# Optimization experiments

Hardware: AMD Instinct MI355X
Metric: run time of the kernel (lower is better)

## Reference

```python
import jax, jax.numpy as jnp
import numpy as np

B, H, KVH, HD, S = 16, 32, 8, 128, 4096
D = H * HD  # 4096
Q = 1  # decode: one query token per batch element


def rotate_half(x):
    half = x.shape[-1] // 2
    return jnp.concatenate([-x[..., half:], x[..., :half]], axis=-1)


def setup_inputs() -> dict:
    key = jax.random.key(0)
    ks = jax.random.split(key, 8)
    hidden_states = jax.random.normal(ks[0], (B, Q, D), dtype=jnp.float32)
    current_steps = jax.random.randint(ks[1], (B,), 0, S - 1)
    # additive causal mask per batch: positions <= current_step visible
    pos = jnp.arange(S)[None, :]
    attention_mask = jnp.where(pos <= current_steps[:, None], 0.0, -1e9).astype(jnp.float32)[:, None, None, :]  # [B,1,1,S]
    # RoPE cos/sin at each batch element's current position
    inv_freq = 1.0 / (10000.0 ** (jnp.arange(0, HD, 2, dtype=jnp.float32) / HD))
    ang = current_steps[:, None].astype(jnp.float32) * inv_freq[None, :]  # [B, HD/2]
    ang = jnp.concatenate([ang, ang], axis=-1)  # [B, HD]
    cos = jnp.cos(ang)[:, None, None, :]  # [B,1,1,HD]
    sin = jnp.sin(ang)[:, None, None, :]
    past_key = jax.random.normal(ks[2], (B, KVH, S, HD), dtype=jnp.float32)
    past_value = jax.random.normal(ks[3], (B, KVH, S, HD), dtype=jnp.float32)
    sc = 1.0 / np.sqrt(D)
    Wq = jax.random.normal(ks[4], (D, H * HD), dtype=jnp.float32) * sc
    Wk = jax.random.normal(ks[5], (D, KVH * HD), dtype=jnp.float32) * sc
    Wv = jax.random.normal(ks[6], (D, KVH * HD), dtype=jnp.float32) * sc
    Wo = jax.random.normal(ks[7], (H * HD, D), dtype=jnp.float32) * sc
    return dict(hidden_states=hidden_states, attention_mask=attention_mask,
                current_steps=current_steps, cos=cos, sin=sin,
                past_key=past_key, past_value=past_value,
                Wq=Wq, Wk=Wk, Wv=Wv, Wo=Wo)


def reference(hidden_states, attention_mask, current_steps, cos, sin,
              past_key, past_value, Wq, Wk, Wv, Wo):
    b, q_len, d = hidden_states.shape
    # projections -> [B, heads, Q, HD]
    q = (hidden_states @ Wq).reshape(b, q_len, H, HD).transpose(0, 2, 1, 3)
    k = (hidden_states @ Wk).reshape(b, q_len, KVH, HD).transpose(0, 2, 1, 3)
    v = (hidden_states @ Wv).reshape(b, q_len, KVH, HD).transpose(0, 2, 1, 3)
    # RoPE
    q = q * cos + rotate_half(q) * sin
    k = k * cos + rotate_half(k) * sin
    # KV-cache scatter at current_step per batch (slice_scatter equivalent)
    def upd(cache_b, new_b, step):
        return jax.lax.dynamic_update_slice(cache_b, new_b, (0, step, 0))
    new_key = jax.vmap(upd)(past_key, k, current_steps)      # [B,KVH,S,HD]
    new_value = jax.vmap(upd)(past_value, v, current_steps)  # [B,KVH,S,HD]
    # GQA attention
    g = H // KVH
    qg = q.reshape(b, KVH, g, q_len, HD)
    scores = jnp.einsum('bkgqd,bksd->bkgqs', qg, new_key) / np.sqrt(HD)
    scores = scores + attention_mask[:, :, None, :, :]  # [B,1,1,Q,S] broadcast
    probs = jax.nn.softmax(scores, axis=-1)
    out = jnp.einsum('bkgqs,bksd->bkgqd', probs, new_value)
    out = out.reshape(b, H, q_len, HD).transpose(0, 2, 1, 3).reshape(b, q_len, H * HD)
    attn_out = out @ Wo
    return attn_out, new_key, new_value
```

## Files before the change

### kernel.cpp

```cpp
#include <hip/hip_runtime.h>

#define B 16
#define H 32
#define KVH 8
#define HD 128
#define S 4096
#define D 4096
#define NQKV 6144
#define PSPLIT 32
#define WSPLIT 32
#define NCH 16
#define CROWS (S / NCH)
#define SCALE 0.08838834764831845f

__global__ void k_proj(const float* __restrict__ hs, const float* __restrict__ Wq,
                       const float* __restrict__ Wk, const float* __restrict__ Wv,
                       float* __restrict__ part) {
  int n = blockIdx.x * 256 + threadIdx.x;
  int k0 = blockIdx.y * (D / PSPLIT);
  const float* w; int ldw, col;
  if (n < 4096)      { w = Wq; ldw = 4096; col = n; }
  else if (n < 5120) { w = Wk; ldw = 1024; col = n - 4096; }
  else               { w = Wv; ldw = 1024; col = n - 5120; }
  float acc[B];
#pragma unroll
  for (int b = 0; b < B; b++) acc[b] = 0.f;
  const float* wp = w + (size_t)k0 * ldw + col;
#pragma unroll 8
  for (int k = 0; k < D / PSPLIT; k++) {
    float wv = wp[(size_t)k * ldw];
#pragma unroll
    for (int b = 0; b < B; b++) acc[b] = fmaf(hs[b * D + k0 + k], wv, acc[b]);
  }
  float* p = part + (size_t)blockIdx.y * (B * NQKV);
#pragma unroll
  for (int b = 0; b < B; b++) p[(size_t)b * NQKV + n] = acc[b];
}

__global__ void k_reduce_rope(const float* __restrict__ part, const float* __restrict__ cosb,
                              const float* __restrict__ sinb, const int* __restrict__ steps,
                              float* __restrict__ qr, float* __restrict__ nkrow,
                              float* __restrict__ nvrow) {
  int i = blockIdx.x * 256 + threadIdx.x;
  int b = i / NQKV, n = i % NQKV;
  float v = 0.f;
#pragma unroll
  for (int c = 0; c < PSPLIT; c++) v += part[(size_t)c * B * NQKV + (size_t)b * NQKV + n];
  if (n < 5120) {
    int d = n & 127;
    int pn = (d < 64) ? n + 64 : n - 64;
    float pv = 0.f;
#pragma unroll
    for (int c = 0; c < PSPLIT; c++) pv += part[(size_t)c * B * NQKV + (size_t)b * NQKV + pn];
    float rot = (d < 64) ? -pv : pv;
    float r = v * cosb[b * HD + d] + rot * sinb[b * HD + d];
    if (n < 4096) qr[(size_t)b * D + n] = r;
    else          nkrow[(size_t)b * KVH * HD + (n - 4096)] = r;
  } else {
    nvrow[(size_t)b * KVH * HD + (n - 5120)] = v;
  }
}

__global__ void k_fusedK(const float* __restrict__ pastk, const float* __restrict__ nkrow,
                         const float* __restrict__ qr, const int* __restrict__ steps,
                         float* __restrict__ newk, float* __restrict__ scores) {
  int ch = blockIdx.x, kvh = blockIdx.y, b = blockIdx.z;
  int t = threadIdx.x;
  __shared__ float4 qs4[128];
  __shared__ float4 ks4[32 * 32];
  int s0 = ch * CROWS;
  int step = steps[b];
  int L = step + 1;
  int h0 = kvh * 4;
  if (t < 128) qs4[t] = ((const float4*)(qr + ((size_t)b * H + h0) * HD))[t];
  float4 subv = ((const float4*)(nkrow + (size_t)(b * KVH + kvh) * HD))[t & 31];
  const float4* src = (const float4*)(pastk + ((size_t)(b * KVH + kvh) * S + s0) * HD);
  float4*       dst = (float4*)(newk + ((size_t)(b * KVH + kvh) * S + s0) * HD);
  int row_c = t & 31, half = (t >> 5) & 1, h = t >> 6;
  float* srow = scores + (size_t)(b * H + h0 + h) * S + s0;
  int d4 = t & 31, r0 = t >> 5;
  float4 v0 = src[t];
  float4 v1 = src[256 + t];
  float4 v2 = src[512 + t];
  float4 v3 = src[768 + t];
  __syncthreads();
  for (int tile = 0; tile < CROWS / 32; ++tile) {
    int rbase = s0 + tile * 32;
    if (rbase + r0      == step) v0 = subv;
    if (rbase + r0 + 8  == step) v1 = subv;
    if (rbase + r0 + 16 == step) v2 = subv;
    if (rbase + r0 + 24 == step) v3 = subv;
    dst[tile * 1024 + t] = v0;
    dst[tile * 1024 + 256 + t] = v1;
    dst[tile * 1024 + 512 + t] = v2;
    dst[tile * 1024 + 768 + t] = v3;
    ks4[r0 * 32        + (d4 ^ (r0 & 7))]        = v0;
    ks4[(r0 + 8) * 32  + (d4 ^ ((r0 + 8) & 7))]  = v1;
    ks4[(r0 + 16) * 32 + (d4 ^ ((r0 + 16) & 7))] = v2;
    ks4[(r0 + 24) * 32 + (d4 ^ ((r0 + 24) & 7))] = v3;
    float4 n0, n1, n2, n3;
    bool more = (tile + 1 < CROWS / 32);
    if (more) {
      n0 = src[(tile + 1) * 1024 + t];
      n1 = src[(tile + 1) * 1024 + 256 + t];
      n2 = src[(tile + 1) * 1024 + 512 + t];
      n3 = src[(tile + 1) * 1024 + 768 + t];
    }
    __syncthreads();
    if (rbase < L) {
      float a0 = 0.f, a1 = 0.f, a2 = 0.f, a3 = 0.f;
      const float4* qp = &qs4[h * 32 + half * 16];
      const float4* kp = &ks4[row_c * 32];
      int sw = row_c & 7;
#pragma unroll
      for (int r = 0; r < 16; r += 4) {
        float4 k0v = kp[(half * 16 + r)     ^ sw], q0v = qp[r];
        float4 k1v = kp[(half * 16 + r + 1) ^ sw], q1v = qp[r + 1];
        float4 k2v = kp[(half * 16 + r + 2) ^ sw], q2v = qp[r + 2];
        float4 k3v = kp[(half * 16 + r + 3) ^ sw], q3v = qp[r + 3];
        a0 = fmaf(k0v.x, q0v.x, fmaf(k0v.y, q0v.y, fmaf(k0v.z, q0v.z, fmaf(k0v.w, q0v.w, a0))));
        a1 = fmaf(k1v.x, q1v.x, fmaf(k1v.y, q1v.y, fmaf(k1v.z, q1v.z, fmaf(k1v.w, q1v.w, a1))));
        a2 = fmaf(k2v.x, q2v.x, fmaf(k2v.y, q2v.y, fmaf(k2v.z, q2v.z, fmaf(k2v.w, q2v.w, a2))));
        a3 = fmaf(k3v.x, q3v.x, fmaf(k3v.y, q3v.y, fmaf(k3v.z, q3v.z, fmaf(k3v.w, q3v.w, a3))));
      }
      float accv = (a0 + a1) + (a2 + a3);
      accv += __shfl_xor(accv, 32);
      if (half == 0) srow[tile * 32 + row_c] = accv * SCALE;
    }
    __syncthreads();
    if (more) { v0 = n0; v1 = n1; v2 = n2; v3 = n3; }
  }
}

__global__ void k_smax(float* __restrict__ scores, const int* __restrict__ steps) {
  int bid = blockIdx.x;
  int b = bid >> 5, h = bid & 31;
  int t = threadIdx.x;
  __shared__ float red[4];
  int L = steps[b] + 1;
  float* srow = scores + (size_t)(b * H + h) * S;
  float lmax = -1e30f;
  for (int s = t; s < L; s += 256) lmax = fmaxf(lmax, srow[s]);
#pragma unroll
  for (int o = 32; o > 0; o >>= 1) lmax = fmaxf(lmax, __shfl_xor(lmax, o));
  if ((t & 63) == 0) red[t >> 6] = lmax;
  __syncthreads();
  float gm = fmaxf(fmaxf(red[0], red[1]), fmaxf(red[2], red[3]));
  float lsum = 0.f;
  for (int s = t; s < L; s += 256) {
    float p = __expf(srow[s] - gm);
    srow[s] = p;
    lsum += p;
  }
#pragma unroll
  for (int o = 32; o > 0; o >>= 1) lsum += __shfl_xor(lsum, o);
  __syncthreads();
  if ((t & 63) == 0) red[t >> 6] = lsum;
  __syncthreads();
  float inv = 1.f / (red[0] + red[1] + red[2] + red[3]);
  for (int s = t; s < L; s += 256) srow[s] *= inv;
}

__global__ void k_fusedV(const float* __restrict__ pastv, const float* __restrict__ nvrow,
                         const float* __restrict__ probs, const int* __restrict__ steps,
                         float* __restrict__ newv, float* __restrict__ part) {
  int ch = blockIdx.x, kvh = blockIdx.y, b = blockIdx.z;
  int t = threadIdx.x;
  int d4 = t & 31, rr = t >> 5;
  int s0 = ch * CROWS;
  int step = steps[b];
  int L = step + 1;
  int h0 = kvh * 4;
  float4 subv = ((const float4*)(nvrow + (size_t)(b * KVH + kvh) * HD))[d4];
  const float4* src = (const float4*)(pastv + ((size_t)(b * KVH + kvh) * S + s0) * HD);
  float4*       dst = (float4*)(newv + ((size_t)(b * KVH + kvh) * S + s0) * HD);
  const float* pb = probs + (size_t)(b * H + h0) * S + s0;
  float4 a0 = make_float4(0.f, 0.f, 0.f, 0.f), a1 = a0, a2 = a0, a3 = a0;
#pragma unroll 4
  for (int i = 0; i < CROWS / 8; ++i) {
    int r = i * 8 + rr;
    float4 v = src[r * 32 + d4];
    if (s0 + r == step) v = subv;
    dst[r * 32 + d4] = v;
    if (s0 + r < L) {
      float q0 = pb[r], q1 = pb[S + r], q2 = pb[2 * S + r], q3 = pb[3 * S + r];
      a0.x = fmaf(q0, v.x, a0.x); a0.y = fmaf(q0, v.y, a0.y);
      a0.z = fmaf(q0, v.z, a0.z); a0.w = fmaf(q0, v.w, a0.w);
      a1.x = fmaf(q1, v.x, a1.x); a1.y = fmaf(q1, v.y, a1.y);
      a1.z = fmaf(q1, v.z, a1.z); a1.w = fmaf(q1, v.w, a1.w);
      a2.x = fmaf(q2, v.x, a2.x); a2.y = fmaf(q2, v.y, a2.y);
      a2.z = fmaf(q2, v.z, a2.z); a2.w = fmaf(q2, v.w, a2.w);
      a3.x = fmaf(q3, v.x, a3.x); a3.y = fmaf(q3, v.y, a3.y);
      a3.z = fmaf(q3, v.z, a3.z); a3.w = fmaf(q3, v.w, a3.w);
    }
  }
#pragma unroll
  for (int c = 0; c < 1; c++) {
    a0.x += __shfl_xor(a0.x, 32); a0.y += __shfl_xor(a0.y, 32);
    a0.z += __shfl_xor(a0.z, 32); a0.w += __shfl_xor(a0.w, 32);
    a1.x += __shfl_xor(a1.x, 32); a1.y += __shfl_xor(a1.y, 32);
    a1.z += __shfl_xor(a1.z, 32); a1.w += __shfl_xor(a1.w, 32);
    a2.x += __shfl_xor(a2.x, 32); a2.y += __shfl_xor(a2.y, 32);
    a2.z += __shfl_xor(a2.z, 32); a2.w += __shfl_xor(a2.w, 32);
    a3.x += __shfl_xor(a3.x, 32); a3.y += __shfl_xor(a3.y, 32);
    a3.z += __shfl_xor(a3.z, 32); a3.w += __shfl_xor(a3.w, 32);
  }
  __shared__ float4 red[4][4][32];
  int w = t >> 6;
  if ((t & 32) == 0) {
    red[w][0][d4] = a0; red[w][1][d4] = a1; red[w][2][d4] = a2; red[w][3][d4] = a3;
  }
  __syncthreads();
  if (t < 128) {
    int hh = t >> 5, dd = t & 31;
    float4 x0 = red[0][hh][dd], x1 = red[1][hh][dd], x2 = red[2][hh][dd], x3 = red[3][hh][dd];
    float4 s;
    s.x = (x0.x + x1.x) + (x2.x + x3.x);
    s.y = (x0.y + x1.y) + (x2.y + x3.y);
    s.z = (x0.z + x1.z) + (x2.z + x3.z);
    s.w = (x0.w + x1.w) + (x2.w + x3.w);
    ((float4*)(part + (((size_t)ch * B + b) * KVH + kvh) * 512))[t] = s;
  }
}

__global__ void k_reduce_ctx(const float* __restrict__ part, float* __restrict__ ctx) {
  int i = blockIdx.x * 256 + threadIdx.x;
  int b = i >> 12, r = i & 4095, h = r >> 7, d = r & 127;
  int kvh = h >> 2, hl = h & 3;
  float s = 0.f;
#pragma unroll
  for (int c = 0; c < NCH; c++)
    s += part[(((size_t)c * B + b) * KVH + kvh) * 512 + hl * 128 + d];
  ctx[i] = s;
}

__global__ void k_wo(const float* __restrict__ ctx, const float* __restrict__ Wo,
                     float* __restrict__ part) {
  int n = blockIdx.x * 256 + threadIdx.x;
  int k0 = blockIdx.y * (D / WSPLIT);
  float acc[B];
#pragma unroll
  for (int b = 0; b < B; b++) acc[b] = 0.f;
  const float* wp = Wo + (size_t)k0 * D + n;
#pragma unroll 8
  for (int k = 0; k < D / WSPLIT; k++) {
    float wv = wp[(size_t)k * D];
#pragma unroll
    for (int b = 0; b < B; b++) acc[b] = fmaf(ctx[b * D + k0 + k], wv, acc[b]);
  }
  float* p = part + (size_t)blockIdx.y * (B * D);
#pragma unroll
  for (int b = 0; b < B; b++) p[(size_t)b * D + n] = acc[b];
}

__global__ void k_reduce_out(const float* __restrict__ part, float* __restrict__ out) {
  int i = blockIdx.x * 256 + threadIdx.x;
  float s = 0.f;
#pragma unroll
  for (int c = 0; c < WSPLIT; c++) s += part[(size_t)c * B * D + i];
  out[i] = s;
}

extern "C" void kernel_launch(void* const* d_in, const int* in_sizes, int n_in,
                              void* d_out, int out_size, void* d_ws, size_t ws_size,
                              hipStream_t stream) {
  const float* hs    = (const float*)d_in[0];
  const int*   steps = (const int*)d_in[2];
  const float* cosb  = (const float*)d_in[3];
  const float* sinb  = (const float*)d_in[4];
  const float* pk    = (const float*)d_in[5];
  const float* pvv   = (const float*)d_in[6];
  const float* Wq    = (const float*)d_in[7];
  const float* Wk    = (const float*)d_in[8];
  const float* Wv    = (const float*)d_in[9];
  const float* Wo    = (const float*)d_in[10];

  float* attn_out = (float*)d_out;
  float* newk = attn_out + (size_t)B * D;
  float* newv = newk + (size_t)B * KVH * S * HD;

  float* ws = (float*)d_ws;
  float* A        = ws;
  float* p_part   = A;
  float* p_scores = A;
  float* p_wopart = A;
  float* p_pvpart = A + 3145728;
  float* p_qr     = p_pvpart + 1048576;
  float* p_nkrow  = p_qr + (size_t)B * D;
  float* p_nvrow  = p_nkrow + (size_t)B * KVH * HD;
  float* p_ctx    = p_nvrow + (size_t)B * KVH * HD;

  hipLaunchKernelGGL(k_proj, dim3(NQKV / 256, PSPLIT), dim3(256), 0, stream,
                     hs, Wq, Wk, Wv, p_part);
  hipLaunchKernelGGL(k_reduce_rope, dim3(B * NQKV / 256), dim3(256), 0, stream,
                     p_part, cosb, sinb, steps, p_qr, p_nkrow, p_nvrow);
  hipLaunchKernelGGL(k_fusedK, dim3(NCH, KVH, B), dim3(256), 0, stream,
                     pk, p_nkrow, p_qr, steps, newk, p_scores);
  hipLaunchKernelGGL(k_smax, dim3(B * H), dim3(256), 0, stream,
                     p_scores, steps);
  hipLaunchKernelGGL(k_fusedV, dim3(NCH, KVH, B), dim3(256), 0, stream,
                     pvv, p_nvrow, p_scores, steps, newv, p_pvpart);
  hipLaunchKernelGGL(k_reduce_ctx, dim3(B * D / 256), dim3(256), 0, stream,
                     p_pvpart, p_ctx);
  hipLaunchKernelGGL(k_wo, dim3(D / 256, WSPLIT), dim3(256), 0, stream,
                     p_ctx, Wo, p_wopart);
  hipLaunchKernelGGL(k_reduce_out, dim3(B * D / 256), dim3(256), 0, stream,
                     p_wopart, attn_out);
}
```

Before: 335.7 us.

## Fuse QK, softmax and PV into a single flash-decoding kernel with split-softmax merge

Replaces the three-kernel K-score / softmax / V-accumulate chain with one flash-style kernel that streams K and V tiles together, keeps online max and sum statistics per chunk, and writes partial outputs plus (m, l) stats. The context reduction then rescales and merges the chunks. This removes the global scores round trip and two launches and overlaps the K and V cache copies. In exchange it adds per-tile shuffles, exps and barriers, and raises register pressure under a launch bound of 256 threads with 4 blocks.

```diff
diff --git a/kernel.cpp b/kernel.cpp
--- a/kernel.cpp
+++ b/kernel.cpp
@@ -11,6 +11,7 @@
 #define WSPLIT 32
 #define NCH 16
 #define CROWS (S / NCH)
+#define NT (CROWS / 32)
 #define SCALE 0.08838834764831845f
 
 __global__ void k_proj(const float* __restrict__ hs, const float* __restrict__ Wq,
@@ -61,57 +62,61 @@
   }
 }
 
-__global__ void k_fusedK(const float* __restrict__ pastk, const float* __restrict__ nkrow,
-                         const float* __restrict__ qr, const int* __restrict__ steps,
-                         float* __restrict__ newk, float* __restrict__ scores) {
+__global__ void __launch_bounds__(256, 4)
+k_flash(const float* __restrict__ pastk, const float* __restrict__ pastv,
+        const float* __restrict__ nkrow, const float* __restrict__ nvrow,
+        const float* __restrict__ qr, const int* __restrict__ steps,
+        float* __restrict__ newk, float* __restrict__ newv,
+        float* __restrict__ part, float* __restrict__ stats) {
   int ch = blockIdx.x, kvh = blockIdx.y, b = blockIdx.z;
   int t = threadIdx.x;
   __shared__ float4 qs4[128];
   __shared__ float4 ks4[32 * 32];
+  __shared__ float pbuf[128];
+  __shared__ float alph[4];
+  __shared__ float4 red[4][4][32];
   int s0 = ch * CROWS;
   int step = steps[b];
   int L = step + 1;
   int h0 = kvh * 4;
   if (t < 128) qs4[t] = ((const float4*)(qr + ((size_t)b * H + h0) * HD))[t];
-  float4 subv = ((const float4*)(nkrow + (size_t)(b * KVH + kvh) * HD))[t & 31];
-  const float4* src = (const float4*)(pastk + ((size_t)(b * KVH + kvh) * S + s0) * HD);
-  float4*       dst = (float4*)(newk + ((size_t)(b * KVH + kvh) * S + s0) * HD);
-  int row_c = t & 31, half = (t >> 5) & 1, h = t >> 6;
-  float* srow = scores + (size_t)(b * H + h0 + h) * S + s0;
-  int d4 = t & 31, r0 = t >> 5;
-  float4 v0 = src[t];
-  float4 v1 = src[256 + t];
-  float4 v2 = src[512 + t];
-  float4 v3 = src[768 + t];
-  __syncthreads();
-  for (int tile = 0; tile < CROWS / 32; ++tile) {
+  int d4 = t & 31, rr = t >> 5;
+  float4 ksub = ((const float4*)(nkrow + (size_t)(b * KVH + kvh) * HD))[d4];
+  float4 vsub = ((const float4*)(nvrow + (size_t)(b * KVH + kvh) * HD))[d4];
+  const float4* srck = (const float4*)(pastk + ((size_t)(b * KVH + kvh) * S + s0) * HD);
+  const float4* srcv = (const float4*)(pastv + ((size_t)(b * KVH + kvh) * S + s0) * HD);
+  float4* dstk = (float4*)(newk + ((size_t)(b * KVH + kvh) * S + s0) * HD);
+  float4* dstv = (float4*)(newv + ((size_t)(b * KVH + kvh) * S + s0) * HD);
+  float m_run = -1e30f, l_run = 0.f;
+  float4 acc0 = make_float4(0.f, 0.f, 0.f, 0.f), acc1 = acc0, acc2 = acc0, acc3 = acc0;
+  float4 kreg[4], vreg[4], kregN[4], vregN[4];
+#pragma unroll
+  for (int j = 0; j < 4; ++j) {
+    kreg[j] = srck[(rr + 8 * j) * 32 + d4];
+    vreg[j] = srcv[(rr + 8 * j) * 32 + d4];
+  }
+  for (int tile = 0; tile < NT; ++tile) {
     int rbase = s0 + tile * 32;
-    if (rbase + r0      == step) v0 = subv;
-    if (rbase + r0 + 8  == step) v1 = subv;
-    if (rbase + r0 + 16 == step) v2 = subv;
-    if (rbase + r0 + 24 == step) v3 = subv;
-    dst[tile * 1024 + t] = v0;
-    dst[tile * 1024 + 256 + t] = v1;
-    dst[tile * 1024 + 512 + t] = v2;
-    dst[tile * 1024 + 768 + t] = v3;
-    ks4[r0 * 32        + (d4 ^ (r0 & 7))]        = v0;
-    ks4[(r0 + 8) * 32  + (d4 ^ ((r0 + 8) & 7))]  = v1;
-    ks4[(r0 + 16) * 32 + (d4 ^ ((r0 + 16) & 7))] = v2;
-    ks4[(r0 + 24) * 32 + (d4 ^ ((r0 + 24) & 7))] = v3;
-    float4 n0, n1, n2, n3;
-    bool more = (tile + 1 < CROWS / 32);
-    if (more) {
-      n0 = src[(tile + 1) * 1024 + t];
-      n1 = src[(tile + 1) * 1024 + 256 + t];
-      n2 = src[(tile + 1) * 1024 + 512 + t];
-      n3 = src[(tile + 1) * 1024 + 768 + t];
-    }
-    __syncthreads();
-    if (rbase < L) {
-      float a0 = 0.f, a1 = 0.f, a2 = 0.f, a3 = 0.f;
+    bool active = (rbase < L);
+#pragma unroll
+    for (int j = 0; j < 4; ++j) {
+      int row = rr + 8 * j;
+      if (rbase + row == step) kreg[j] = ksub;
+      dstk[tile * 1024 + row * 32 + d4] = kreg[j];
+      if (active) ks4[row * 32 + (d4 ^ (row & 7))] = kreg[j];
+    }
+    if (tile + 1 < NT) {
+#pragma unroll
+      for (int j = 0; j < 4; ++j)
+        kregN[j] = srck[(tile + 1) * 1024 + (rr + 8 * j) * 32 + d4];
+    }
+    if (active) {
+      __syncthreads();
+      int row_c = t & 31, half = (t >> 5) & 1, h = t >> 6;
       const float4* qp = &qs4[h * 32 + half * 16];
       const float4* kp = &ks4[row_c * 32];
       int sw = row_c & 7;
+      float a0 = 0.f, a1 = 0.f, a2 = 0.f, a3 = 0.f;
 #pragma unroll
       for (int r = 0; r < 16; r += 4) {
         float4 k0v = kp[(half * 16 + r)     ^ sw], q0v = qp[r];
@@ -125,113 +130,109 @@
       }
       float accv = (a0 + a1) + (a2 + a3);
       accv += __shfl_xor(accv, 32);
-      if (half == 0) srow[tile * 32 + row_c] = accv * SCALE;
-    }
-    __syncthreads();
-    if (more) { v0 = n0; v1 = n1; v2 = n2; v3 = n3; }
-  }
-}
-
-__global__ void k_smax(float* __restrict__ scores, const int* __restrict__ steps) {
-  int bid = blockIdx.x;
-  int b = bid >> 5, h = bid & 31;
-  int t = threadIdx.x;
-  __shared__ float red[4];
-  int L = steps[b] + 1;
-  float* srow = scores + (size_t)(b * H + h) * S;
-  float lmax = -1e30f;
-  for (int s = t; s < L; s += 256) lmax = fmaxf(lmax, srow[s]);
-#pragma unroll
-  for (int o = 32; o > 0; o >>= 1) lmax = fmaxf(lmax, __shfl_xor(lmax, o));
-  if ((t & 63) == 0) red[t >> 6] = lmax;
-  __syncthreads();
-  float gm = fmaxf(fmaxf(red[0], red[1]), fmaxf(red[2], red[3]));
-  float lsum = 0.f;
-  for (int s = t; s < L; s += 256) {
-    float p = __expf(srow[s] - gm);
-    srow[s] = p;
-    lsum += p;
-  }
-#pragma unroll
-  for (int o = 32; o > 0; o >>= 1) lsum += __shfl_xor(lsum, o);
-  __syncthreads();
-  if ((t & 63) == 0) red[t >> 6] = lsum;
-  __syncthreads();
-  float inv = 1.f / (red[0] + red[1] + red[2] + red[3]);
-  for (int s = t; s < L; s += 256) srow[s] *= inv;
-}
-
-__global__ void k_fusedV(const float* __restrict__ pastv, const float* __restrict__ nvrow,
-                         const float* __restrict__ probs, const int* __restrict__ steps,
-                         float* __restrict__ newv, float* __restrict__ part) {
-  int ch = blockIdx.x, kvh = blockIdx.y, b = blockIdx.z;
-  int t = threadIdx.x;
-  int d4 = t & 31, rr = t >> 5;
-  int s0 = ch * CROWS;
-  int step = steps[b];
-  int L = step + 1;
-  int h0 = kvh * 4;
-  float4 subv = ((const float4*)(nvrow + (size_t)(b * KVH + kvh) * HD))[d4];
-  const float4* src = (const float4*)(pastv + ((size_t)(b * KVH + kvh) * S + s0) * HD);
-  float4*       dst = (float4*)(newv + ((size_t)(b * KVH + kvh) * S + s0) * HD);
-  const float* pb = probs + (size_t)(b * H + h0) * S + s0;
-  float4 a0 = make_float4(0.f, 0.f, 0.f, 0.f), a1 = a0, a2 = a0, a3 = a0;
-#pragma unroll 4
-  for (int i = 0; i < CROWS / 8; ++i) {
-    int r = i * 8 + rr;
-    float4 v = src[r * 32 + d4];
-    if (s0 + r == step) v = subv;
-    dst[r * 32 + d4] = v;
-    if (s0 + r < L) {
-      float q0 = pb[r], q1 = pb[S + r], q2 = pb[2 * S + r], q3 = pb[3 * S + r];
-      a0.x = fmaf(q0, v.x, a0.x); a0.y = fmaf(q0, v.y, a0.y);
-      a0.z = fmaf(q0, v.z, a0.z); a0.w = fmaf(q0, v.w, a0.w);
-      a1.x = fmaf(q1, v.x, a1.x); a1.y = fmaf(q1, v.y, a1.y);
-      a1.z = fmaf(q1, v.z, a1.z); a1.w = fmaf(q1, v.w, a1.w);
-      a2.x = fmaf(q2, v.x, a2.x); a2.y = fmaf(q2, v.y, a2.y);
-      a2.z = fmaf(q2, v.z, a2.z); a2.w = fmaf(q2, v.w, a2.w);
-      a3.x = fmaf(q3, v.x, a3.x); a3.y = fmaf(q3, v.y, a3.y);
-      a3.z = fmaf(q3, v.z, a3.z); a3.w = fmaf(q3, v.w, a3.w);
-    }
-  }
-#pragma unroll
-  for (int c = 0; c < 1; c++) {
-    a0.x += __shfl_xor(a0.x, 32); a0.y += __shfl_xor(a0.y, 32);
-    a0.z += __shfl_xor(a0.z, 32); a0.w += __shfl_xor(a0.w, 32);
-    a1.x += __shfl_xor(a1.x, 32); a1.y += __shfl_xor(a1.y, 32);
-    a1.z += __shfl_xor(a1.z, 32); a1.w += __shfl_xor(a1.w, 32);
-    a2.x += __shfl_xor(a2.x, 32); a2.y += __shfl_xor(a2.y, 32);
-    a2.z += __shfl_xor(a2.z, 32); a2.w += __shfl_xor(a2.w, 32);
-    a3.x += __shfl_xor(a3.x, 32); a3.y += __shfl_xor(a3.y, 32);
-    a3.z += __shfl_xor(a3.z, 32); a3.w += __shfl_xor(a3.w, 32);
-  }
-  __shared__ float4 red[4][4][32];
+      float s = accv * SCALE;
+      if (rbase + row_c >= L) s = -1e30f;
+      float tmax = s;
+#pragma unroll
+      for (int o = 1; o < 32; o <<= 1) tmax = fmaxf(tmax, __shfl_xor(tmax, o));
+      float mnew = fmaxf(m_run, tmax);
+      float p = __expf(s - mnew);
+      float psum = p;
+#pragma unroll
+      for (int o = 1; o < 32; o <<= 1) psum += __shfl_xor(psum, o);
+      float alpha = __expf(m_run - mnew);
+      l_run = l_run * alpha + psum;
+      m_run = mnew;
+      pbuf[h * 32 + row_c] = p;
+      if ((t & 63) == 0) alph[h] = alpha;
+      __syncthreads();
+    }
+#pragma unroll
+    for (int j = 0; j < 4; ++j) {
+      int row = rr + 8 * j;
+      if (rbase + row == step) vreg[j] = vsub;
+      dstv[tile * 1024 + row * 32 + d4] = vreg[j];
+    }
+    if (tile + 1 < NT) {
+#pragma unroll
+      for (int j = 0; j < 4; ++j)
+        vregN[j] = srcv[(tile + 1) * 1024 + (rr + 8 * j) * 32 + d4];
+    }
+    if (active) {
+      float al0 = alph[0], al1 = alph[1], al2 = alph[2], al3 = alph[3];
+      acc0.x *= al0; acc0.y *= al0; acc0.z *= al0; acc0.w *= al0;
+      acc1.x *= al1; acc1.y *= al1; acc1.z *= al1; acc1.w *= al1;
+      acc2.x *= al2; acc2.y *= al2; acc2.z *= al2; acc2.w *= al2;
+      acc3.x *= al3; acc3.y *= al3; acc3.z *= al3; acc3.w *= al3;
+#pragma unroll
+      for (int j = 0; j < 4; ++j) {
+        int row = rr + 8 * j;
+        float p0 = pbuf[row], p1 = pbuf[32 + row], p2 = pbuf[64 + row], p3 = pbuf[96 + row];
+        float4 v = vreg[j];
+        acc0.x = fmaf(p0, v.x, acc0.x); acc0.y = fmaf(p0, v.y, acc0.y);
+        acc0.z = fmaf(p0, v.z, acc0.z); acc0.w = fmaf(p0, v.w, acc0.w);
+        acc1.x = fmaf(p1, v.x, acc1.x); acc1.y = fmaf(p1, v.y, acc1.y);
+        acc1.z = fmaf(p1, v.z, acc1.z); acc1.w = fmaf(p1, v.w, acc1.w);
+        acc2.x = fmaf(p2, v.x, acc2.x); acc2.y = fmaf(p2, v.y, acc2.y);
+        acc2.z = fmaf(p2, v.z, acc2.z); acc2.w = fmaf(p2, v.w, acc2.w);
+        acc3.x = fmaf(p3, v.x, acc3.x); acc3.y = fmaf(p3, v.y, acc3.y);
+        acc3.z = fmaf(p3, v.z, acc3.z); acc3.w = fmaf(p3, v.w, acc3.w);
+      }
+    }
+    if (tile + 1 < NT) {
+#pragma unroll
+      for (int j = 0; j < 4; ++j) { kreg[j] = kregN[j]; vreg[j] = vregN[j]; }
+    }
+  }
+  acc0.x += __shfl_xor(acc0.x, 32); acc0.y += __shfl_xor(acc0.y, 32);
+  acc0.z += __shfl_xor(acc0.z, 32); acc0.w += __shfl_xor(acc0.w, 32);
+  acc1.x += __shfl_xor(acc1.x, 32); acc1.y += __shfl_xor(acc1.y, 32);
+  acc1.z += __shfl_xor(acc1.z, 32); acc1.w += __shfl_xor(acc1.w, 32);
+  acc2.x += __shfl_xor(acc2.x, 32); acc2.y += __shfl_xor(acc2.y, 32);
+  acc2.z += __shfl_xor(acc2.z, 32); acc2.w += __shfl_xor(acc2.w, 32);
+  acc3.x += __shfl_xor(acc3.x, 32); acc3.y += __shfl_xor(acc3.y, 32);
+  acc3.z += __shfl_xor(acc3.z, 32); acc3.w += __shfl_xor(acc3.w, 32);
   int w = t >> 6;
   if ((t & 32) == 0) {
-    red[w][0][d4] = a0; red[w][1][d4] = a1; red[w][2][d4] = a2; red[w][3][d4] = a3;
+    red[w][0][d4] = acc0; red[w][1][d4] = acc1;
+    red[w][2][d4] = acc2; red[w][3][d4] = acc3;
   }
   __syncthreads();
   if (t < 128) {
     int hh = t >> 5, dd = t & 31;
     float4 x0 = red[0][hh][dd], x1 = red[1][hh][dd], x2 = red[2][hh][dd], x3 = red[3][hh][dd];
-    float4 s;
-    s.x = (x0.x + x1.x) + (x2.x + x3.x);
-    s.y = (x0.y + x1.y) + (x2.y + x3.y);
-    s.z = (x0.z + x1.z) + (x2.z + x3.z);
-    s.w = (x0.w + x1.w) + (x2.w + x3.w);
-    ((float4*)(part + (((size_t)ch * B + b) * KVH + kvh) * 512))[t] = s;
-  }
-}
-
-__global__ void k_reduce_ctx(const float* __restrict__ part, float* __restrict__ ctx) {
+    float4 sv;
+    sv.x = (x0.x + x1.x) + (x2.x + x3.x);
+    sv.y = (x0.y + x1.y) + (x2.y + x3.y);
+    sv.z = (x0.z + x1.z) + (x2.z + x3.z);
+    sv.w = (x0.w + x1.w) + (x2.w + x3.w);
+    ((float4*)(part + (((size_t)ch * B + b) * KVH + kvh) * 512))[t] = sv;
+  }
+  if ((t & 63) == 0) {
+    size_t si = ((((size_t)ch * B + b) * KVH + kvh) * 4 + w) * 2;
+    stats[si] = m_run;
+    stats[si + 1] = l_run;
+  }
+}
+
+__global__ void k_reduce_ctx(const float* __restrict__ part, const float* __restrict__ stats,
+                             float* __restrict__ ctx) {
   int i = blockIdx.x * 256 + threadIdx.x;
   int b = i >> 12, r = i & 4095, h = r >> 7, d = r & 127;
   int kvh = h >> 2, hl = h & 3;
-  float s = 0.f;
+  float M = -1e30f;
 #pragma unroll
   for (int c = 0; c < NCH; c++)
-    s += part[(((size_t)c * B + b) * KVH + kvh) * 512 + hl * 128 + d];
-  ctx[i] = s;
+    M = fmaxf(M, stats[((((size_t)c * B + b) * KVH + kvh) * 4 + hl) * 2]);
+  float num = 0.f, den = 0.f;
+#pragma unroll
+  for (int c = 0; c < NCH; c++) {
+    size_t si = ((((size_t)c * B + b) * KVH + kvh) * 4 + hl) * 2;
+    float wgt = __expf(stats[si] - M);
+    den += wgt * stats[si + 1];
+    num += wgt * part[(((size_t)c * B + b) * KVH + kvh) * 512 + hl * 128 + d];
+  }
+  ctx[i] = num / den;
 }
 
 __global__ void k_wo(const float* __restrict__ ctx, const float* __restrict__ Wo,
@@ -282,10 +283,10 @@
   float* ws = (float*)d_ws;
   float* A        = ws;
   float* p_part   = A;
-  float* p_scores = A;
   float* p_wopart = A;
   float* p_pvpart = A + 3145728;
-  float* p_qr     = p_pvpart + 1048576;
+  float* p_stats  = p_pvpart + 1048576;
+  float* p_qr     = p_stats + 16384;
   float* p_nkrow  = p_qr + (size_t)B * D;
   float* p_nvrow  = p_nkrow + (size_t)B * KVH * HD;
   float* p_ctx    = p_nvrow + (size_t)B * KVH * HD;
@@ -294,14 +295,11 @@
                      hs, Wq, Wk, Wv, p_part);
   hipLaunchKernelGGL(k_reduce_rope, dim3(B * NQKV / 256), dim3(256), 0, stream,
                      p_part, cosb, sinb, steps, p_qr, p_nkrow, p_nvrow);
-  hipLaunchKernelGGL(k_fusedK, dim3(NCH, KVH, B), dim3(256), 0, stream,
-                     pk, p_nkrow, p_qr, steps, newk, p_scores);
-  hipLaunchKernelGGL(k_smax, dim3(B * H), dim3(256), 0, stream,
-                     p_scores, steps);
-  hipLaunchKernelGGL(k_fusedV, dim3(NCH, KVH, B), dim3(256), 0, stream,
-                     pvv, p_nvrow, p_scores, steps, newv, p_pvpart);
+  hipLaunchKernelGGL(k_flash, dim3(NCH, KVH, B), dim3(256), 0, stream,
+                     pk, pvv, p_nkrow, p_nvrow, p_qr, steps, newk, newv,
+                     p_pvpart, p_stats);
   hipLaunchKernelGGL(k_reduce_ctx, dim3(B * D / 256), dim3(256), 0, stream,
-                     p_pvpart, p_ctx);
+                     p_pvpart, p_stats, p_ctx);
   hipLaunchKernelGGL(k_wo, dim3(D / 256, WSPLIT), dim3(256), 0, stream,
                      p_ctx, Wo, p_wopart);
   hipLaunchKernelGGL(k_reduce_out, dim3(B * D / 256), dim3(256), 0, stream,
```

Result: slower. 350.5 us (+4.4%).

## Compute QK scores from registers without LDS staging or block barriers

Applied to the files above, without the earlier changes.

The fused K-cache copy and score kernel no longer stages K tiles and Q in shared memory behind two barriers per tile. Each group of 16 lanes now owns one key row: it loads the row straight from global memory, writes it to the new cache, keeps the four query heads in registers, and reduces the dot products with shuffles across 16 lanes. The goal is to drop the LDS traffic and synchronisation stalls, at the cost of more shuffle work per row, more registers for Q, and losing the explicit next-tile prefetch. The value-kernel shuffle loop is only unwrapped, with no behaviour change.

```diff
diff --git a/kernel.cpp b/kernel.cpp
--- a/kernel.cpp
+++ b/kernel.cpp
@@ -66,69 +66,54 @@
                          float* __restrict__ newk, float* __restrict__ scores) {
   int ch = blockIdx.x, kvh = blockIdx.y, b = blockIdx.z;
   int t = threadIdx.x;
-  __shared__ float4 qs4[128];
-  __shared__ float4 ks4[32 * 32];
+  int ln = t & 15, rg = t >> 4;
   int s0 = ch * CROWS;
   int step = steps[b];
   int L = step + 1;
   int h0 = kvh * 4;
-  if (t < 128) qs4[t] = ((const float4*)(qr + ((size_t)b * H + h0) * HD))[t];
-  float4 subv = ((const float4*)(nkrow + (size_t)(b * KVH + kvh) * HD))[t & 31];
+  const float4* qbase = (const float4*)(qr + ((size_t)b * H + h0) * HD);
+  float4 q0[4], q1[4];
+#pragma unroll
+  for (int h = 0; h < 4; h++) {
+    q0[h] = qbase[h * 32 + ln];
+    q1[h] = qbase[h * 32 + ln + 16];
+  }
+  const float4* subp = (const float4*)(nkrow + (size_t)(b * KVH + kvh) * HD);
+  float4 sub0 = subp[ln], sub1 = subp[ln + 16];
   const float4* src = (const float4*)(pastk + ((size_t)(b * KVH + kvh) * S + s0) * HD);
   float4*       dst = (float4*)(newk + ((size_t)(b * KVH + kvh) * S + s0) * HD);
-  int row_c = t & 31, half = (t >> 5) & 1, h = t >> 6;
-  float* srow = scores + (size_t)(b * H + h0 + h) * S + s0;
-  int d4 = t & 31, r0 = t >> 5;
-  float4 v0 = src[t];
-  float4 v1 = src[256 + t];
-  float4 v2 = src[512 + t];
-  float4 v3 = src[768 + t];
-  __syncthreads();
-  for (int tile = 0; tile < CROWS / 32; ++tile) {
-    int rbase = s0 + tile * 32;
-    if (rbase + r0      == step) v0 = subv;
-    if (rbase + r0 + 8  == step) v1 = subv;
-    if (rbase + r0 + 16 == step) v2 = subv;
-    if (rbase + r0 + 24 == step) v3 = subv;
-    dst[tile * 1024 + t] = v0;
-    dst[tile * 1024 + 256 + t] = v1;
-    dst[tile * 1024 + 512 + t] = v2;
-    dst[tile * 1024 + 768 + t] = v3;
-    ks4[r0 * 32        + (d4 ^ (r0 & 7))]        = v0;
-    ks4[(r0 + 8) * 32  + (d4 ^ ((r0 + 8) & 7))]  = v1;
-    ks4[(r0 + 16) * 32 + (d4 ^ ((r0 + 16) & 7))] = v2;
-    ks4[(r0 + 24) * 32 + (d4 ^ ((r0 + 24) & 7))] = v3;
-    float4 n0, n1, n2, n3;
-    bool more = (tile + 1 < CROWS / 32);
-    if (more) {
-      n0 = src[(tile + 1) * 1024 + t];
-      n1 = src[(tile + 1) * 1024 + 256 + t];
-      n2 = src[(tile + 1) * 1024 + 512 + t];
-      n3 = src[(tile + 1) * 1024 + 768 + t];
+  float* srow = scores + (size_t)(b * H + h0) * S + s0;
+#pragma unroll 4
+  for (int it = 0; it < CROWS / 16; ++it) {
+    int row = it * 16 + rg;
+    size_t o0 = (size_t)row * 32 + ln;
+    float4 k0 = src[o0];
+    float4 k1 = src[o0 + 16];
+    if (s0 + row == step) { k0 = sub0; k1 = sub1; }
+    dst[o0] = k0;
+    dst[o0 + 16] = k1;
+    if (s0 + row < L) {
+      float a0, a1, a2, a3;
+      a0 = fmaf(k0.x, q0[0].x, fmaf(k0.y, q0[0].y, fmaf(k0.z, q0[0].z, fmaf(k0.w, q0[0].w,
+           fmaf(k1.x, q1[0].x, fmaf(k1.y, q1[0].y, fmaf(k1.z, q1[0].z, k1.w * q1[0].w)))))));
+      a1 = fmaf(k0.x, q0[1].x, fmaf(k0.y, q0[1].y, fmaf(k0.z, q0[1].z, fmaf(k0.w, q0[1].w,
+           fmaf(k1.x, q1[1].x, fmaf(k1.y, q1[1].y, fmaf(k1.z, q1[1].z, k1.w * q1[1].w)))))));
+      a2 = fmaf(k0.x, q0[2].x, fmaf(k0.y, q0[2].y, fmaf(k0.z, q0[2].z, fmaf(k0.w, q0[2].w,
+           fmaf(k1.x, q1[2].x, fmaf(k1.y, q1[2].y, fmaf(k1.z, q1[2].z, k1.w * q1[2].w)))))));
+      a3 = fmaf(k0.x, q0[3].x, fmaf(k0.y, q0[3].y, fmaf(k0.z, q0[3].z, fmaf(k0.w, q0[3].w,
+           fmaf(k1.x, q1[3].x, fmaf(k1.y, q1[3].y, fmaf(k1.z, q1[3].z, k1.w * q1[3].w)))))));
+#pragma unroll
+      for (int o = 1; o < 16; o <<= 1) {
+        a0 += __shfl_xor(a0, o);
+        a1 += __shfl_xor(a1, o);
+        a2 += __shfl_xor(a2, o);
+        a3 += __shfl_xor(a3, o);
+      }
+      if (ln < 4) {
+        float my = (ln == 0) ? a0 : (ln == 1) ? a1 : (ln == 2) ? a2 : a3;
+        srow[(size_t)ln * S + row] = my * SCALE;
+      }
     }
-    __syncthreads();
-    if (rbase < L) {
-      float a0 = 0.f, a1 = 0.f, a2 = 0.f, a3 = 0.f;
-      const float4* qp = &qs4[h * 32 + half * 16];
-      const float4* kp = &ks4[row_c * 32];
-      int sw = row_c & 7;
-#pragma unroll
-      for (int r = 0; r < 16; r += 4) {
-        float4 k0v = kp[(half * 16 + r)     ^ sw], q0v = qp[r];
-        float4 k1v = kp[(half * 16 + r + 1) ^ sw], q1v = qp[r + 1];
-        float4 k2v = kp[(half * 16 + r + 2) ^ sw], q2v = qp[r + 2];
-        float4 k3v = kp[(half * 16 + r + 3) ^ sw], q3v = qp[r + 3];
-        a0 = fmaf(k0v.x, q0v.x, fmaf(k0v.y, q0v.y, fmaf(k0v.z, q0v.z, fmaf(k0v.w, q0v.w, a0))));
-        a1 = fmaf(k1v.x, q1v.x, fmaf(k1v.y, q1v.y, fmaf(k1v.z, q1v.z, fmaf(k1v.w, q1v.w, a1))));
-        a2 = fmaf(k2v.x, q2v.x, fmaf(k2v.y, q2v.y, fmaf(k2v.z, q2v.z, fmaf(k2v.w, q2v.w, a2))));
-        a3 = fmaf(k3v.x, q3v.x, fmaf(k3v.y, q3v.y, fmaf(k3v.z, q3v.z, fmaf(k3v.w, q3v.w, a3))));
-      }
-      float accv = (a0 + a1) + (a2 + a3);
-      accv += __shfl_xor(accv, 32);
-      if (half == 0) srow[tile * 32 + row_c] = accv * SCALE;
-    }
-    __syncthreads();
-    if (more) { v0 = n0; v1 = n1; v2 = n2; v3 = n3; }
   }
 }
 
@@ -194,17 +179,14 @@
       a3.z = fmaf(q3, v.z, a3.z); a3.w = fmaf(q3, v.w, a3.w);
     }
   }
-#pragma unroll
-  for (int c = 0; c < 1; c++) {
-    a0.x += __shfl_xor(a0.x, 32); a0.y += __shfl_xor(a0.y, 32);
-    a0.z += __shfl_xor(a0.z, 32); a0.w += __shfl_xor(a0.w, 32);
-    a1.x += __shfl_xor(a1.x, 32); a1.y += __shfl_xor(a1.y, 32);
-    a1.z += __shfl_xor(a1.z, 32); a1.w += __shfl_xor(a1.w, 32);
-    a2.x += __shfl_xor(a2.x, 32); a2.y += __shfl_xor(a2.y, 32);
-    a2.z += __shfl_xor(a2.z, 32); a2.w += __shfl_xor(a2.w, 32);
-    a3.x += __shfl_xor(a3.x, 32); a3.y += __shfl_xor(a3.y, 32);
-    a3.z += __shfl_xor(a3.z, 32); a3.w += __shfl_xor(a3.w, 32);
-  }
+  a0.x += __shfl_xor(a0.x, 32); a0.y += __shfl_xor(a0.y, 32);
+  a0.z += __shfl_xor(a0.z, 32); a0.w += __shfl_xor(a0.w, 32);
+  a1.x += __shfl_xor(a1.x, 32); a1.y += __shfl_xor(a1.y, 32);
+  a1.z += __shfl_xor(a1.z, 32); a1.w += __shfl_xor(a1.w, 32);
+  a2.x += __shfl_xor(a2.x, 32); a2.y += __shfl_xor(a2.y, 32);
+  a2.z += __shfl_xor(a2.z, 32); a2.w += __shfl_xor(a2.w, 32);
+  a3.x += __shfl_xor(a3.x, 32); a3.y += __shfl_xor(a3.y, 32);
+  a3.z += __shfl_xor(a3.z, 32); a3.w += __shfl_xor(a3.w, 32);
   __shared__ float4 red[4][4][32];
   int w = t >> 6;
   if ((t & 32) == 0) {
```

Measured after the change: 343.4 us. 2.3% more time.
